# Optimization experiments

Measured on AMD Instinct MI355X. Metric: run time of the kernel, lower is better.

The kernel has to match this reference:

```python
import jax, jax.numpy as jnp
import numpy as np

B, S, E = 4, 2048, 2048
N_HEADS, HEAD_DIM = 16, 128
NHD = N_HEADS * HEAD_DIM  # n_heads_dim == emb_dim here


def setup_inputs() -> dict:
    key = jax.random.key(0)
    ks = jax.random.split(key, 7)
    s = 0.02
    return {
        "x": jax.random.normal(ks[0], (B, S, E), dtype=jnp.float32),
        # torch nn.Linear weights: [out_features, in_features]
        "w_q": jax.random.normal(ks[1], (NHD, E), dtype=jnp.float32) * s,
        "w_k": jax.random.normal(ks[2], (NHD, E), dtype=jnp.float32) * s,
        "w_v": jax.random.normal(ks[3], (NHD, E), dtype=jnp.float32) * s,
        "w_proj": jax.random.normal(ks[4], (E, NHD), dtype=jnp.float32) * s,
        "b_proj": jax.random.normal(ks[5], (E,), dtype=jnp.float32) * s,
    }


def reference(x, w_q, w_k, w_v, w_proj, b_proj):
    b, s, _ = x.shape
    # projections (torch Linear: y = x @ W^T) -> [b, s, n_heads, head_dim] -> [b, h, s, d]
    def split_heads(y):
        return y.reshape(b, s, N_HEADS, HEAD_DIM).transpose(0, 2, 1, 3)
    q = split_heads(x @ w_q.T)
    k = split_heads(x @ w_k.T)
    v = split_heads(x @ w_v.T)
    scale = 1.0 / np.sqrt(HEAD_DIM).astype(np.float32)
    scores = jnp.einsum("bhsd,bhtd->bhst", q, k) * scale  # [b, h, s, s]
    causal = jnp.tril(jnp.ones((s, s), dtype=bool))
    scores = jnp.where(causal, scores, jnp.finfo(scores.dtype).min)
    attn = jax.nn.softmax(scores, axis=-1)
    out = jnp.einsum("bhst,bhtd->bhsd", attn, v)  # [b, h, s, d]
    out = out.transpose(0, 2, 1, 3).reshape(b, s, NHD)
    return out @ w_proj.T + b_proj
```

## Files before the change

kernel.cpp:

```cpp
#include <hip/hip_runtime.h>

#define LOG2E 1.4426950408889634f
#define ATTN_SCALE 0.08838834764831843f

using bhalf8 = __attribute__((ext_vector_type(8))) short;
using f32x4  = __attribute__((ext_vector_type(4))) float;

__device__ __forceinline__ unsigned short f2bf(float f) {
  unsigned u = __float_as_uint(f);
  u += 0x7fffu + ((u >> 16) & 1u);
  return (unsigned short)(u >> 16);
}

__device__ __forceinline__ unsigned pack_bf16_2(float lo, float hi) {
  unsigned a = __float_as_uint(lo) + 0x8000u;
  unsigned b = __float_as_uint(hi) + 0x8000u;
  return __builtin_amdgcn_perm(b, a, 0x07060302);
}

__device__ __forceinline__ void gl_lds16(const unsigned short* g, unsigned short* l) {
  __builtin_amdgcn_global_load_lds(
      (const __attribute__((address_space(1))) void*)g,
      (__attribute__((address_space(3))) void*)l, 16, 0, 0);
}

__global__ void cvt_kernel(const float* __restrict__ src,
                           unsigned short* __restrict__ dst, int n4) {
  int i = blockIdx.x * blockDim.x + threadIdx.x;
  if (i >= n4) return;
  float4 f = reinterpret_cast<const float4*>(src)[i];
  unsigned lo = (unsigned)f2bf(f.x) | ((unsigned)f2bf(f.y) << 16);
  unsigned hi = (unsigned)f2bf(f.z) | ((unsigned)f2bf(f.w) << 16);
  reinterpret_cast<uint2*>(dst)[i] = make_uint2(lo, hi);
}

#define GBAR()  asm volatile("s_barrier" ::: "memory")
#define GWAITL() do { asm volatile("s_waitcnt lgkmcnt(0)" ::: "memory"); \
                      __builtin_amdgcn_sched_barrier(0); } while (0)

__device__ __forceinline__ bhalf8 ldsfrag(const unsigned short* b, int rb, int kk,
                                          int rbase) {
  return *reinterpret_cast<const bhalf8*>(b + rb * 1024 + kk * 512 + rbase);
}

template <int MODE, int I0, int J0>
__device__ __forceinline__ void mfmaq(f32x4 (&acc)[8][4], const bhalf8 (&afr)[4][2],
                                      const bhalf8 (&bfr)[2][2]) {
#pragma unroll
  for (int i = 0; i < 4; ++i)
#pragma unroll
    for (int j = 0; j < 2; ++j)
#pragma unroll
      for (int kk = 0; kk < 2; ++kk) {
        if (MODE == 1)
          acc[I0 + i][J0 + j] = __builtin_amdgcn_mfma_f32_16x16x32_bf16(
              bfr[j][kk], afr[i][kk], acc[I0 + i][J0 + j], 0, 0, 0);
        else
          acc[I0 + i][J0 + j] = __builtin_amdgcn_mfma_f32_16x16x32_bf16(
              afr[i][kk], bfr[j][kk], acc[I0 + i][J0 + j], 0, 0, 0);
      }
}

__device__ __forceinline__ void stage_half(const unsigned short* __restrict__ M,
                                           unsigned short* dstbase, int h, int ks,
                                           int rowb, int wave, const int (&rdec)[2],
                                           const int (&cdec)[2]) {
#pragma unroll
  for (int ld = 0; ld < 2; ++ld)
    gl_lds16(M + (size_t)(rowb + rdec[ld] + h * 128) * 2048 + ks + cdec[ld],
             dstbase + h * 8192 + ld * 4096 + wave * 512);
}

template <int MODE>
__device__ __forceinline__ void ktile256(
    const unsigned short* __restrict__ A, const unsigned short* __restrict__ Bt,
    unsigned short* as_, unsigned short* bs_, int ks,
    int row0, int col0, int wave, int wr, int wc, int rbase,
    const int (&rdec)[2], const int (&cdec)[2],
    f32x4 (&acc)[8][4], bhalf8 (&af)[4][2], bhalf8 (&bfA)[2][2], bhalf8 (&bfB)[2][2]) {
#pragma unroll
  for (int i = 0; i < 4; ++i)
#pragma unroll
    for (int kk = 0; kk < 2; ++kk) af[i][kk] = ldsfrag(as_, wr * 8 + i, kk, rbase);
#pragma unroll
  for (int j = 0; j < 2; ++j)
#pragma unroll
    for (int kk = 0; kk < 2; ++kk) bfA[j][kk] = ldsfrag(bs_, wc * 4 + j, kk, rbase);
  GBAR(); GWAITL();
  __builtin_amdgcn_s_setprio(1);
  mfmaq<MODE, 0, 0>(acc, af, bfA);
  __builtin_amdgcn_s_setprio(0);
  GBAR();
#pragma unroll
  for (int j = 0; j < 2; ++j)
#pragma unroll
    for (int kk = 0; kk < 2; ++kk) bfB[j][kk] = ldsfrag(bs_, wc * 4 + 2 + j, kk, rbase);
  GBAR(); GWAITL();
  __builtin_amdgcn_s_setprio(1);
  mfmaq<MODE, 0, 2>(acc, af, bfB);
  __builtin_amdgcn_s_setprio(0);
  GBAR();
#pragma unroll
  for (int i = 0; i < 4; ++i)
#pragma unroll
    for (int kk = 0; kk < 2; ++kk) af[i][kk] = ldsfrag(as_, wr * 8 + 4 + i, kk, rbase);
  stage_half(Bt, bs_, 0, ks, col0, wave, rdec, cdec);
  GBAR(); GWAITL();
  __builtin_amdgcn_s_setprio(1);
  mfmaq<MODE, 4, 2>(acc, af, bfB);
  __builtin_amdgcn_s_setprio(0);
  GBAR();
  stage_half(Bt, bs_, 1, ks, col0, wave, rdec, cdec);
  stage_half(A,  as_, 0, ks, row0, wave, rdec, cdec);
  stage_half(A,  as_, 1, ks, row0, wave, rdec, cdec);
  GBAR();
  __builtin_amdgcn_s_setprio(1);
  mfmaq<MODE, 4, 0>(acc, af, bfA);
  __builtin_amdgcn_s_setprio(0);
  asm volatile("s_waitcnt vmcnt(8)" ::: "memory");
  GBAR();
}

template <int MODE>
__global__ __launch_bounds__(512, 2) void gemm256_bt(
    const unsigned short* __restrict__ A,
    const unsigned short* __restrict__ Bt,
    unsigned short* __restrict__ obf, float* __restrict__ of32,
    const float* __restrict__ bias) {
  __shared__ __align__(16) unsigned short As[2][16384];
  __shared__ __align__(16) unsigned short Bs[2][16384];
  const int tid  = threadIdx.x;
  const int lane = tid & 63;
  const int wave = tid >> 6;
  const int quad = lane >> 4;
  const int c16  = lane & 15;
  const int wr = wave >> 2, wc = wave & 3;
  const int row0 = blockIdx.y * 256;
  const int col0 = blockIdx.x * 256;

  const int rbase = c16 * 32 + ((quad * 8) ^ ((c16 >> 3) << 4));

  int rdec[2], cdec[2];
#pragma unroll
  for (int ld = 0; ld < 2; ++ld) {
    const int c = ld * 512 + tid;
    rdec[ld] = ((c >> 7) << 4) + ((c >> 2) & 15);
    cdec[ld] = (((c >> 6) & 1) << 5) + (((c & 3) << 3) ^ (((c >> 5) & 1) << 4));
  }

  f32x4 acc[8][4];
#pragma unroll
  for (int i = 0; i < 8; ++i)
#pragma unroll
    for (int j = 0; j < 4; ++j)
#pragma unroll
      for (int r = 0; r < 4; ++r) acc[i][j][r] = 0.0f;

  bhalf8 af[4][2], bfA[2][2], bfB[2][2];

  stage_half(Bt, Bs[0], 0, 0,  col0, wave, rdec, cdec);
  stage_half(Bt, Bs[0], 1, 0,  col0, wave, rdec, cdec);
  stage_half(A,  As[0], 0, 0,  row0, wave, rdec, cdec);
  stage_half(A,  As[0], 1, 0,  row0, wave, rdec, cdec);
  stage_half(Bt, Bs[1], 0, 64, col0, wave, rdec, cdec);
  stage_half(Bt, Bs[1], 1, 64, col0, wave, rdec, cdec);
  stage_half(A,  As[1], 0, 64, row0, wave, rdec, cdec);
  stage_half(A,  As[1], 1, 64, row0, wave, rdec, cdec);
  asm volatile("s_waitcnt vmcnt(8)" ::: "memory");
  GBAR();

#pragma unroll 1
  for (int it = 0; it < 16; ++it) {
    const int kA  = it * 128;
    const int ksA = (kA + 128 > 1984) ? 1984 : kA + 128;
    const int ksB = (kA + 192 > 1984) ? 1984 : kA + 192;
    ktile256<MODE>(A, Bt, As[0], Bs[0], ksA, row0, col0, wave, wr, wc, rbase,
                   rdec, cdec, acc, af, bfA, bfB);
    ktile256<MODE>(A, Bt, As[1], Bs[1], ksB, row0, col0, wave, wr, wc, rbase,
                   rdec, cdec, acc, af, bfA, bfB);
  }

#pragma unroll
  for (int i = 0; i < 8; ++i)
#pragma unroll
    for (int j = 0; j < 4; ++j)
#pragma unroll
      for (int r = 0; r < 4; ++r) {
        float v = acc[i][j][r];
        if (MODE == 2) {
          int m = row0 + wr * 128 + i * 16 + quad * 4 + r;
          int n = col0 + wc * 64 + j * 16 + c16;
          of32[(size_t)m * 2048 + n] = v + bias[n];
        } else if (MODE == 0) {
          int m = row0 + wr * 128 + i * 16 + quad * 4 + r;
          int n = col0 + wc * 64 + j * 16 + c16;
          int b = m >> 11, s = m & 2047;
          int h = n >> 7,  d = n & 127;
          obf[(((size_t)(b * 16 + h)) * 2048 + s) * 128 + d] = f2bf(v);
        } else {
          int n = col0 + wc * 64 + j * 16 + quad * 4 + r;
          int m = row0 + wr * 128 + i * 16 + c16;
          int b = m >> 11, s = m & 2047;
          int h = n >> 7,  d = n & 127;
          obf[(((size_t)(b * 16 + h)) * 128 + d) * 2048 + s] = f2bf(v);
        }
      }
}

#define LQK 136
#define LV   72
__global__ __launch_bounds__(256, 4) void flash_kernel(
    const unsigned short* __restrict__ Q,
    const unsigned short* __restrict__ K,
    const unsigned short* __restrict__ Vt,
    unsigned short* __restrict__ O) {
  const int tid  = threadIdx.x;
  const int lane = tid & 63;
  const int wave = tid >> 6;
  const int quad = lane >> 4;
  const int c16  = lane & 15;
  const int bh = blockIdx.x;
  const int q0 = (31 - blockIdx.y) * 64;
  const int bb = bh >> 4, hh = bh & 15;
  const int qidx = q0 + wave * 16 + c16;
  const float SL = ATTN_SCALE * LOG2E;

  __shared__ __align__(16) unsigned short Ks[64 * LQK];
  __shared__ __align__(16) unsigned short Vs[128 * LV];

  const unsigned short* Qg = Q + ((size_t)bh * 2048 + q0) * 128;
#pragma unroll
  for (int i = 0; i < 4; i++) {
    int chunk = i * 256 + tid;
    int t = chunk >> 4, dc = (chunk & 15) << 3;
    *reinterpret_cast<bhalf8*>(Ks + t * LQK + dc) =
        *reinterpret_cast<const bhalf8*>(Qg + chunk * 8);
  }
  __syncthreads();
  bhalf8 qb[4];
#pragma unroll
  for (int kk = 0; kk < 4; kk++)
    qb[kk] = *reinterpret_cast<const bhalf8*>(Ks + (wave * 16 + c16) * LQK + kk * 32 + quad * 8);

  f32x4 o_acc[8];
#pragma unroll
  for (int jd = 0; jd < 8; jd++)
#pragma unroll
    for (int r = 0; r < 4; r++) o_acc[jd][r] = 0.0f;
  float m_i = -__builtin_inff(), l_i = 0.0f;

  const unsigned short* Kbh = K  + (size_t)bh * 2048 * 128;
  const unsigned short* Vbh = Vt + (size_t)bh * 128 * 2048;

  const int nt = q0 / 64 + 1;
  for (int it = 0; it < nt; ++it) {
    const int t0 = it * 64;
    bhalf8 rk[4], rv[4];
#pragma unroll
    for (int i = 0; i < 4; i++) {
      int chunk = i * 256 + tid;
      int t = chunk >> 4, dc = (chunk & 15) << 3;
      rk[i] = *reinterpret_cast<const bhalf8*>(Kbh + (size_t)(t0 + t) * 128 + dc);
      int d = chunk >> 3, tc = (chunk & 7) << 3;
      rv[i] = *reinterpret_cast<const bhalf8*>(Vbh + (size_t)d * 2048 + t0 + tc);
    }
    __syncthreads();
#pragma unroll
    for (int i = 0; i < 4; i++) {
      int chunk = i * 256 + tid;
      int t = chunk >> 4, dc = (chunk & 15) << 3;
      int row = (((t >> 5) << 1) | ((t >> 2) & 1)) * 16 + ((t >> 3) & 3) * 4 + (t & 3);
      *reinterpret_cast<bhalf8*>(Ks + row * LQK + dc) = rk[i];
      int d = chunk >> 3, tc = (chunk & 7) << 3;
      *reinterpret_cast<bhalf8*>(Vs + d * LV + tc) = rv[i];
    }
    __syncthreads();

    f32x4 st[4];
#pragma unroll
    for (int tt = 0; tt < 4; tt++) {
#pragma unroll
      for (int r = 0; r < 4; r++) st[tt][r] = 0.0f;
#pragma unroll
      for (int kk = 0; kk < 4; kk++) {
        bhalf8 ka = *reinterpret_cast<const bhalf8*>(Ks + (tt * 16 + c16) * LQK + kk * 32 + quad * 8);
        st[tt] = __builtin_amdgcn_mfma_f32_16x16x32_bf16(ka, qb[kk], st[tt], 0, 0, 0);
      }
    }

    const bool diag = (t0 == q0);
    float pv[4][4];
    float tmax = m_i;
#pragma unroll
    for (int tt = 0; tt < 4; tt++)
#pragma unroll
      for (int r = 0; r < 4; r++) {
        float x = st[tt][r] * SL;
        if (diag) {
          int t = t0 + ((tt >> 1) << 5) + (quad << 3) + ((tt & 1) << 2) + r;
          if (t > qidx) x = -__builtin_inff();
        }
        pv[tt][r] = x;
        tmax = fmaxf(tmax, x);
      }
    tmax = fmaxf(tmax, __shfl_xor(tmax, 16));
    tmax = fmaxf(tmax, __shfl_xor(tmax, 32));
    const float alpha = exp2f(m_i - tmax);
    m_i = tmax;
    float rs = 0.0f;
#pragma unroll
    for (int tt = 0; tt < 4; tt++)
#pragma unroll
      for (int r = 0; r < 4; r++) {
        float p = exp2f(pv[tt][r] - m_i);
        pv[tt][r] = p;
        rs += p;
      }
    l_i = l_i * alpha + rs;
#pragma unroll
    for (int jd = 0; jd < 8; jd++)
#pragma unroll
      for (int r = 0; r < 4; r++) o_acc[jd][r] *= alpha;

#pragma unroll
    for (int u = 0; u < 2; u++) {
      union { bhalf8 h; uint4 w; } pu;
      pu.w.x = pack_bf16_2(pv[2 * u][0],     pv[2 * u][1]);
      pu.w.y = pack_bf16_2(pv[2 * u][2],     pv[2 * u][3]);
      pu.w.z = pack_bf16_2(pv[2 * u + 1][0], pv[2 * u + 1][1]);
      pu.w.w = pack_bf16_2(pv[2 * u + 1][2], pv[2 * u + 1][3]);
#pragma unroll
      for (int jd = 0; jd < 8; jd++) {
        bhalf8 va = *reinterpret_cast<const bhalf8*>(Vs + (jd * 16 + c16) * LV + u * 32 + quad * 8);
        o_acc[jd] = __builtin_amdgcn_mfma_f32_16x16x32_bf16(va, pu.h, o_acc[jd], 0, 0, 0);
      }
    }
  }

  l_i += __shfl_xor(l_i, 16);
  l_i += __shfl_xor(l_i, 32);
  const float inv = 1.0f / l_i;
#pragma unroll
  for (int jd = 0; jd < 8; jd++) {
    unsigned lo = (unsigned)f2bf(o_acc[jd][0] * inv) | ((unsigned)f2bf(o_acc[jd][1] * inv) << 16);
    unsigned hi = (unsigned)f2bf(o_acc[jd][2] * inv) | ((unsigned)f2bf(o_acc[jd][3] * inv) << 16);
    *reinterpret_cast<uint2*>(O + ((size_t)(bb * 2048 + qidx)) * 2048 + hh * 128 + jd * 16 + quad * 4) =
        make_uint2(lo, hi);
  }
}

extern "C" void kernel_launch(void* const* d_in, const int* in_sizes, int n_in,
                              void* d_out, int out_size, void* d_ws, size_t ws_size,
                              hipStream_t stream) {
  const float* x  = (const float*)d_in[0];
  const float* wq = (const float*)d_in[1];
  const float* wk = (const float*)d_in[2];
  const float* wv = (const float*)d_in[3];
  const float* wp = (const float*)d_in[4];
  const float* bp = (const float*)d_in[5];
  float* out = (float*)d_out;

  unsigned short* ws  = (unsigned short*)d_ws;
  const size_t ME = (size_t)8192 * 2048;
  const size_t EE = (size_t)2048 * 2048;
  unsigned short* xb  = ws;
  unsigned short* wqb = xb  + ME;
  unsigned short* wkb = wqb + EE;
  unsigned short* wvb = wkb + EE;
  unsigned short* wpb = wvb + EE;
  unsigned short* Qb  = wpb + EE;
  unsigned short* Kb  = Qb  + ME;
  unsigned short* Vtb = Kb  + ME;
  unsigned short* Ob  = Vtb + ME;

  cvt_kernel<<<16384, 256, 0, stream>>>(x,  xb,  (int)(ME / 4));
  cvt_kernel<<<4096,  256, 0, stream>>>(wq, wqb, (int)(EE / 4));
  cvt_kernel<<<4096,  256, 0, stream>>>(wk, wkb, (int)(EE / 4));
  cvt_kernel<<<4096,  256, 0, stream>>>(wv, wvb, (int)(EE / 4));
  cvt_kernel<<<4096,  256, 0, stream>>>(wp, wpb, (int)(EE / 4));

  dim3 g2(8, 32);
  gemm256_bt<0><<<g2, 512, 0, stream>>>(xb, wqb, Qb,  nullptr, nullptr);
  gemm256_bt<0><<<g2, 512, 0, stream>>>(xb, wkb, Kb,  nullptr, nullptr);
  gemm256_bt<1><<<g2, 512, 0, stream>>>(xb, wvb, Vtb, nullptr, nullptr);

  flash_kernel<<<dim3(64, 32), 256, 0, stream>>>(Qb, Kb, Vtb, Ob);

  gemm256_bt<2><<<g2, 512, 0, stream>>>(Ob, wpb, nullptr, out, bp);
}
```

Measured before the change: 615.0 us.

## Prefetch next K/V tile in registers, lazy softmax rescale, XCD-aware GEMM tile mapping

The attention kernel now double-buffers K/V global loads in registers, issuing the next tile's loads right after the LDS store so their latency overlaps the QK and PV MFMAs. Softmax rescaling of the accumulator is skipped unless a wave's row max grows by more than 8 (log2 units), and the scale is folded into an FMA inside exp2. The GEMM remaps block IDs so each XCD works on a contiguous band of output rows, aiming for better L2 reuse. The register double buffer adds pressure that may lower occupancy, and lazy rescaling allows larger intermediate values in fp32 and bf16-packed probabilities.

```diff
diff --git a/kernel.cpp b/kernel.cpp
--- a/kernel.cpp
+++ b/kernel.cpp
@@ -135,8 +135,12 @@
   const int quad = lane >> 4;
   const int c16  = lane & 15;
   const int wr = wave >> 2, wc = wave & 3;
-  const int row0 = blockIdx.y * 256;
-  const int col0 = blockIdx.x * 256;
+
+  const int wg  = blockIdx.y * 8 + blockIdx.x;
+  const int xcd = wg & 7;
+  const int idx = wg >> 3;
+  const int row0 = (xcd * 4 + (idx >> 3)) * 256;
+  const int col0 = (idx & 7) * 256;
 
   const int rbase = c16 * 32 + ((quad * 8) ^ ((c16 >> 3) << 4));
 
@@ -228,6 +232,23 @@
   __shared__ __align__(16) unsigned short Ks[64 * LQK];
   __shared__ __align__(16) unsigned short Vs[128 * LV];
 
+  const unsigned short* Kbh = K  + (size_t)bh * 2048 * 128;
+  const unsigned short* Vbh = Vt + (size_t)bh * 128 * 2048;
+  const int nt = q0 / 64 + 1;
+
+  bhalf8 rkA[4], rvA[4], rkB[4], rvB[4];
+  auto fl_load = [&](int t0, bhalf8 (&rk)[4], bhalf8 (&rv)[4]) {
+#pragma unroll
+    for (int i = 0; i < 4; i++) {
+      int chunk = i * 256 + tid;
+      int t = chunk >> 4, dc = (chunk & 15) << 3;
+      rk[i] = *reinterpret_cast<const bhalf8*>(Kbh + (size_t)(t0 + t) * 128 + dc);
+      int d = chunk >> 3, tc = (chunk & 7) << 3;
+      rv[i] = *reinterpret_cast<const bhalf8*>(Vbh + (size_t)d * 2048 + t0 + tc);
+    }
+  };
+  fl_load(0, rkA, rvA);
+
   const unsigned short* Qg = Q + ((size_t)bh * 2048 + q0) * 128;
 #pragma unroll
   for (int i = 0; i < 4; i++) {
@@ -249,21 +270,9 @@
     for (int r = 0; r < 4; r++) o_acc[jd][r] = 0.0f;
   float m_i = -__builtin_inff(), l_i = 0.0f;
 
-  const unsigned short* Kbh = K  + (size_t)bh * 2048 * 128;
-  const unsigned short* Vbh = Vt + (size_t)bh * 128 * 2048;
-
-  const int nt = q0 / 64 + 1;
-  for (int it = 0; it < nt; ++it) {
+  auto tile = [&](bhalf8 (&rk)[4], bhalf8 (&rv)[4],
+                  bhalf8 (&nk)[4], bhalf8 (&nv)[4], int it) {
     const int t0 = it * 64;
-    bhalf8 rk[4], rv[4];
-#pragma unroll
-    for (int i = 0; i < 4; i++) {
-      int chunk = i * 256 + tid;
-      int t = chunk >> 4, dc = (chunk & 15) << 3;
-      rk[i] = *reinterpret_cast<const bhalf8*>(Kbh + (size_t)(t0 + t) * 128 + dc);
-      int d = chunk >> 3, tc = (chunk & 7) << 3;
-      rv[i] = *reinterpret_cast<const bhalf8*>(Vbh + (size_t)d * 2048 + t0 + tc);
-    }
     __syncthreads();
 #pragma unroll
     for (int i = 0; i < 4; i++) {
@@ -276,6 +285,8 @@
     }
     __syncthreads();
 
+    if (it + 1 < nt) fl_load(t0 + 64, nk, nv);
+
     f32x4 st[4];
 #pragma unroll
     for (int tt = 0; tt < 4; tt++) {
@@ -290,37 +301,44 @@
 
     const bool diag = (t0 == q0);
     float pv[4][4];
-    float tmax = m_i;
+    float rmax = -__builtin_inff();
 #pragma unroll
     for (int tt = 0; tt < 4; tt++)
 #pragma unroll
       for (int r = 0; r < 4; r++) {
-        float x = st[tt][r] * SL;
+        float x = st[tt][r];
         if (diag) {
           int t = t0 + ((tt >> 1) << 5) + (quad << 3) + ((tt & 1) << 2) + r;
           if (t > qidx) x = -__builtin_inff();
         }
         pv[tt][r] = x;
-        tmax = fmaxf(tmax, x);
-      }
-    tmax = fmaxf(tmax, __shfl_xor(tmax, 16));
-    tmax = fmaxf(tmax, __shfl_xor(tmax, 32));
-    const float alpha = exp2f(m_i - tmax);
-    m_i = tmax;
+        rmax = fmaxf(rmax, x);
+      }
+    rmax = fmaxf(rmax, __shfl_xor(rmax, 16));
+    rmax = fmaxf(rmax, __shfl_xor(rmax, 32));
+    const float pmax_s = rmax * SL;
+
+    if (__any(pmax_s > m_i + 8.0f)) {
+      const float mnew = fmaxf(m_i, pmax_s);
+      const float alpha = exp2f(m_i - mnew);
+      m_i = mnew;
+      l_i *= alpha;
+#pragma unroll
+      for (int jd = 0; jd < 8; jd++)
+#pragma unroll
+        for (int r = 0; r < 4; r++) o_acc[jd][r] *= alpha;
+    }
+
     float rs = 0.0f;
 #pragma unroll
     for (int tt = 0; tt < 4; tt++)
 #pragma unroll
       for (int r = 0; r < 4; r++) {
-        float p = exp2f(pv[tt][r] - m_i);
+        float p = exp2f(__builtin_fmaf(pv[tt][r], SL, -m_i));
         pv[tt][r] = p;
         rs += p;
       }
-    l_i = l_i * alpha + rs;
-#pragma unroll
-    for (int jd = 0; jd < 8; jd++)
-#pragma unroll
-      for (int r = 0; r < 4; r++) o_acc[jd][r] *= alpha;
+    l_i += rs;
 
 #pragma unroll
     for (int u = 0; u < 2; u++) {
@@ -335,6 +353,15 @@
         o_acc[jd] = __builtin_amdgcn_mfma_f32_16x16x32_bf16(va, pu.h, o_acc[jd], 0, 0, 0);
       }
     }
+  };
+
+  int it = 0;
+#pragma unroll 1
+  for (;;) {
+    tile(rkA, rvA, rkB, rvB, it);
+    if (++it == nt) break;
+    tile(rkB, rvB, rkA, rvA, it);
+    if (++it == nt) break;
   }
 
   l_i += __shfl_xor(l_i, 16);
```

Result: slower. 774.6 us (+26.0%).
